# Kernel optimization log

Hardware: AMD Instinct MI355X
Metric: run time of the kernel (lower is better)

The kernel has to match this reference:

```python
import jax, jax.numpy as jnp
import numpy as np

# ---- circuit constants (E / Opcode) ----
D = 16            # E.DIM
P = 8             # E.NUM_POSITIONS (32 bits as 8 nibbles)
S = 100.0         # E.SCALE
POS, NIB_A, NIB_B, RESULT, CARRY_IN, CARRY_OUT, TEMP = 0, 1, 2, 3, 4, 5, 6
OPMUL = 10        # E.OP_START(=8) + Opcode.MUL(=2)
B = 131072        # batch of independent multiply circuits


def _bake():
    f = np.float32
    p = {}
    # MulInitAccumulatorFFN (hidden 2)
    Wu0 = np.zeros((2, D), f); bu0 = np.zeros(2, f)
    Wg0 = np.zeros((2, D), f); bg0 = np.zeros(2, f)
    Wd0 = np.zeros((D, 2), f)
    Wu0[0, OPMUL] = S;  Wg0[0, RESULT] = -1.0; Wd0[RESULT, 0] = 1.0 / S
    Wu0[1, OPMUL] = -S; Wg0[1, RESULT] = 1.0;  Wd0[RESULT, 1] = 1.0 / S
    p.update(Wu0=Wu0, bu0=bu0, Wg0=Wg0, bg0=bg0, Wd0=Wd0)
    # ExtractBitFFN(i) (hidden 4) and ShiftedAddFFN(i) (hidden 16), i in 0..31
    Wu_e = np.zeros((32, 4, D), f); bu_e = np.zeros((32, 4), f)
    Wg_e = np.zeros((32, 4, D), f); bg_e = np.zeros((32, 4), f)
    Wd_e = np.zeros((32, D, 4), f)
    Wu_s = np.zeros((32, 16, D), f); bu_s = np.zeros((32, 16), f)
    Wg_s = np.zeros((32, 16, D), f); bg_s = np.zeros((32, 16), f)
    Wd_s = np.zeros((32, D, 16), f)
    for i in range(32):
        npos, bit = i // 4, i % 4
        Wu_e[i, 0, POS] = S
        bu_e[i, 0] = -S * (npos - 0.5)
        Wg_e[i, 0, NIB_B] = 1.0 / float(1 << bit)
        Wd_e[i, TEMP, 0] = 1.0 / S
        mult = float(1 << bit)
        for k in range(P):
            src = k - npos
            if 0 <= src < P:
                r = 2 * k
                Wu_s[i, r, POS] = S
                bu_s[i, r] = -S * (k - 0.5)
                Wg_s[i, r, CARRY_IN] = 1.0
                Wg_s[i, r, NIB_A] = mult
                Wd_s[i, RESULT, r] = 1.0 / S
    p.update(Wu_e=Wu_e, bu_e=bu_e, Wg_e=Wg_e, bg_e=bg_e, Wd_e=Wd_e,
             Wu_s=Wu_s, bu_s=bu_s, Wg_s=Wg_s, bg_s=bg_s, Wd_s=Wd_s)
    # MulAccumulatorCarryFFN (hidden 32) -- identical for all 32 iterations
    Wu_c = np.zeros((32, D), f); bu_c = np.zeros(32, f)
    Wg_c = np.zeros((32, D), f); bg_c = np.zeros(32, f)
    Wd_c = np.zeros((D, 32), f)
    for k in range(1, 16):
        thr = float(k * 16); r = (k - 1) * 2
        Wu_c[r, RESULT] = S;     bu_c[r] = -S * (thr - 1.0)
        Wg_c[r, OPMUL] = 1.0
        Wd_c[RESULT, r] = -16.0 / S; Wd_c[CARRY_OUT, r] = 1.0 / S
        Wu_c[r + 1, RESULT] = S; bu_c[r + 1] = -S * thr
        Wg_c[r + 1, OPMUL] = 1.0
        Wd_c[RESULT, r + 1] = 16.0 / S; Wd_c[CARRY_OUT, r + 1] = -1.0 / S
    p.update(Wu_c=Wu_c, bu_c=bu_c, Wg_c=Wg_c, bg_c=bg_c, Wd_c=Wd_c)
    return p


def setup_inputs() -> dict:
    key = jax.random.key(0)
    x = jax.random.uniform(key, (B, P, D), dtype=jnp.float32)
    # POS channel holds each token's position index (the circuit thresholds on it)
    x = x.at[..., POS].set(jnp.broadcast_to(jnp.arange(P, dtype=jnp.float32), (B, P)))
    params = {k: jnp.asarray(v) for k, v in _bake().items()}
    return {"x": x, **params}


def _ffn(x, Wu, bu, Wg, bg, Wd):
    # PureFFN: residual gated FFN, relu up-projection, linear gate
    h = jax.nn.relu(jnp.einsum('bpd,hd->bph', x, Wu) + bu) \
        * (jnp.einsum('bpd,hd->bph', x, Wg) + bg)
    return x + jnp.einsum('bph,dh->bpd', h, Wd)


def reference(x, Wu0, bu0, Wg0, bg0, Wd0,
              Wu_e, bu_e, Wg_e, bg_e, Wd_e,
              Wu_s, bu_s, Wg_s, bg_s, Wd_s,
              Wu_c, bu_c, Wg_c, bg_c, Wd_c):
    x = _ffn(x, Wu0, bu0, Wg0, bg0, Wd0)  # init accumulator

    def step(c, per_iter):
        wue, bue, wge, bge, wde, wus, bus, wgs, bgs, wds = per_iter
        c = _ffn(c, wue, bue, wge, bge, wde)   # extract bit i of B
        c = _ffn(c, wus, bus, wgs, bgs, wds)   # RESULT += A << i if bit set
        c = _ffn(c, Wu_c, bu_c, Wg_c, bg_c, Wd_c)  # carry propagation
        return c, None

    x, _ = jax.lax.scan(step, x,
                        (Wu_e, bu_e, Wg_e, bg_e, Wd_e,
                         Wu_s, bu_s, Wg_s, bg_s, Wd_s))
    return x
```

## Files before the change

### kernel.cpp

```cpp
#include <hip/hip_runtime.h>


#define TOK_THREADS 256

__global__ __launch_bounds__(TOK_THREADS) void pure_mul32_kernel(
    const float* __restrict__ x, float* __restrict__ out, int ntok) {
  int idx = blockIdx.x * blockDim.x + threadIdx.x;
  if (idx >= ntok) return;

  const float4* __restrict__ xin = reinterpret_cast<const float4*>(x) + (size_t)idx * 4;
  float4 v0 = xin[0];
  float4 v1 = xin[1];
  float4 v2 = xin[2];
  float4 v3 = xin[3];

  const float p  = (float)(idx & 7);
  const float a  = v2.z;
  const float na = v0.y;
  const float nb = v0.z;
  const float ci = v1.x;

  float r  = fmaf(-a, v0.w, v0.w);
  float co = v1.y;
  float t  = v1.z;

  t = fmaf(nb * 0.9375f, (p + 1.f) * (p + 1.f), t);

  const float g0 = ci + na;
  const float g1 = fmaf(2.f, na, ci);
  const float g2 = fmaf(4.f, na, ci);
  const float g3 = fmaf(8.f, na, ci);

#pragma unroll
  for (int npos = 0; npos < 8; ++npos) {
    const float d = p - (float)npos + 1.f;
    const float T = (d > 0.f) ? 0.5f * d * d : 0.f;
#pragma unroll
    for (int bit = 0; bit < 4; ++bit) {
      const float g = (bit == 0) ? g0 : (bit == 1) ? g1 : (bit == 2) ? g2 : g3;
      r = fmaf(g, T, r);
      const float c    = floorf(r * 0.0625f);
      const float full = fminf(c, 15.f);
      float ramp = fminf(fmaxf(fmaf(-16.f, c, r) - 15.f, 0.f), 1.f);
      ramp = (c < 15.f) ? ramp : 0.f;
      const float f = full + ramp;
      r  = fmaf(-16.f * a, f, r);
      co = fmaf(a, f, co);
    }
  }

  v0.w = r;
  v1.y = co;
  v1.z = t;

  float4* __restrict__ o = reinterpret_cast<float4*>(out) + (size_t)idx * 4;
  o[0] = v0; o[1] = v1; o[2] = v2; o[3] = v3;
}

extern "C" void kernel_launch(void* const* d_in, const int* in_sizes, int n_in,
                              void* d_out, int out_size, void* d_ws, size_t ws_size,
                              hipStream_t stream) {
  const float* x = (const float*)d_in[0];
  float* out = (float*)d_out;
  const int ntok = in_sizes[0] / 16;
  const int blocks = (ntok + TOK_THREADS - 1) / TOK_THREADS;
  pure_mul32_kernel<<<blocks, TOK_THREADS, 0, stream>>>(x, out, ntok);
}
```

Before: 155.3 us.

## Map one float4 per thread with wave shuffles for coalesced token I/O

Instead of each thread loading four float4s of one token, each thread now loads a single float4 and the four lanes of a token exchange the needed fields via __shfl. This makes global loads and stores fully coalesced across a wave, at the cost of four times as many threads, each running the full 32-step compute redundantly. The carry-out accumulation is also deferred by summing f and applying a single fma at the end.

New measurement: 156.4 us. No clear change (+0.8%).

```diff
diff --git a/kernel.cpp b/kernel.cpp
--- a/kernel.cpp
+++ b/kernel.cpp
@@ -4,25 +4,26 @@
 #define TOK_THREADS 256
 
 __global__ __launch_bounds__(TOK_THREADS) void pure_mul32_kernel(
-    const float* __restrict__ x, float* __restrict__ out, int ntok) {
-  int idx = blockIdx.x * blockDim.x + threadIdx.x;
-  if (idx >= ntok) return;
+    const float4* __restrict__ x, float4* __restrict__ out, int n4) {
+  const int i = blockIdx.x * TOK_THREADS + threadIdx.x;
+  if (i >= n4) return;
 
-  const float4* __restrict__ xin = reinterpret_cast<const float4*>(x) + (size_t)idx * 4;
-  float4 v0 = xin[0];
-  float4 v1 = xin[1];
-  float4 v2 = xin[2];
-  float4 v3 = xin[3];
+  float4 v = x[i];
 
-  const float p  = (float)(idx & 7);
-  const float a  = v2.z;
-  const float na = v0.y;
-  const float nb = v0.z;
-  const float ci = v1.x;
+  const int lane = threadIdx.x & 63;
+  const int base = lane & ~3;
 
-  float r  = fmaf(-a, v0.w, v0.w);
-  float co = v1.y;
-  float t  = v1.z;
+  const float na = __shfl(v.y, base);
+  const float nb = __shfl(v.z, base);
+  const float r0 = __shfl(v.w, base);
+  const float ci = __shfl(v.x, base + 1);
+  float co       = __shfl(v.y, base + 1);
+  float t        = __shfl(v.z, base + 1);
+  const float a  = __shfl(v.z, base + 2);
+
+  const float p = (float)((i >> 2) & 7);
+
+  float r = fmaf(-a, r0, r0);
 
   t = fmaf(nb * 0.9375f, (p + 1.f) * (p + 1.f), t);
 
@@ -30,6 +31,9 @@
   const float g1 = fmaf(2.f, na, ci);
   const float g2 = fmaf(4.f, na, ci);
   const float g3 = fmaf(8.f, na, ci);
+  const float m  = -16.f * a;
+
+  float fs = 0.f;
 
 #pragma unroll
   for (int npos = 0; npos < 8; ++npos) {
@@ -44,25 +48,29 @@
       float ramp = fminf(fmaxf(fmaf(-16.f, c, r) - 15.f, 0.f), 1.f);
       ramp = (c < 15.f) ? ramp : 0.f;
       const float f = full + ramp;
-      r  = fmaf(-16.f * a, f, r);
-      co = fmaf(a, f, co);
+      r  = fmaf(m, f, r);
+      fs += f;
     }
   }
+  co = fmaf(a, fs, co);
 
-  v0.w = r;
-  v1.y = co;
-  v1.z = t;
+  const int sub = lane & 3;
+  if (sub == 0) {
+    v.w = r;
+  } else if (sub == 1) {
+    v.y = co;
+    v.z = t;
+  }
 
-  float4* __restrict__ o = reinterpret_cast<float4*>(out) + (size_t)idx * 4;
-  o[0] = v0; o[1] = v1; o[2] = v2; o[3] = v3;
+  out[i] = v;
 }
 
 extern "C" void kernel_launch(void* const* d_in, const int* in_sizes, int n_in,
                               void* d_out, int out_size, void* d_ws, size_t ws_size,
                               hipStream_t stream) {
-  const float* x = (const float*)d_in[0];
-  float* out = (float*)d_out;
-  const int ntok = in_sizes[0] / 16;
-  const int blocks = (ntok + TOK_THREADS - 1) / TOK_THREADS;
-  pure_mul32_kernel<<<blocks, TOK_THREADS, 0, stream>>>(x, out, ntok);
+  const float4* x = (const float4*)d_in[0];
+  float4* out = (float4*)d_out;
+  const int n4 = in_sizes[0] / 4;
+  const int blocks = (n4 + TOK_THREADS - 1) / TOK_THREADS;
+  pure_mul32_kernel<<<blocks, TOK_THREADS, 0, stream>>>(x, out, n4);
 }
```
